# Performance work log

Hardware: AMD Instinct MI355X
Metric: run time of the kernel (lower is better)

Reference implementation:

```python
import jax, jax.numpy as jnp
import numpy as np

MUL0, MUL1 = 64, 32          # 64x0e + 32x1e irreps_emb
D_FEAT = MUL0 + 3 * MUL1     # 160
N_T, N_Q, N_K = 64, 1024, 1024


def quat_apply(q, v):
    # q: (...,4) real-first (w,x,y,z); v: (...,3). Rotate v by q.
    w = q[..., :1]
    u = q[..., 1:]
    uv = jnp.cross(u, v)
    return v + 2.0 * (w * uv + jnp.cross(u, uv))


def split_irreps(f):
    # f: (..., 160) -> scalars (...,64), vectors (...,32,3)
    s = f[..., :MUL0]
    v = f[..., MUL0:].reshape(f.shape[:-1] + (MUL1, 3))
    return s, v


def dtp(a, b, Ws, Wv):
    # Depthwise tensor product restricted to l<=1 (SeparableFCTP analogue),
    # output irreps 1x0e + 32x1e, with SiLU activation on the scalar part.
    sa, va = split_irreps(a)
    sb, vb = split_irreps(b)
    # scalar paths: 0e*0e and 1e.1e (dot) -> 96 scalar channels
    scal = jnp.concatenate([sa * sb, jnp.einsum('...ci,...ci->...c', va, vb)], axis=-1)
    # vector paths: 0e*1e, 1e*0e, 1e x 1e (cross) -> 96 vector channels
    vec = jnp.concatenate(
        [sa[..., :MUL1, None] * vb, va * sb[..., :MUL1, None], jnp.cross(va, vb)], axis=-2)
    out_s = jax.nn.silu(scal @ Ws)                    # (...,1)
    out_v = jnp.einsum('...ci,co->...oi', vec, Wv)    # (...,32,3)
    return out_s, out_v


def get_key_features(points, key_coord, key_feat, W_key):
    # radius-style key lookup: nearest key node + smooth radial envelope + linear
    d2 = jnp.sum((points[:, None, :] - key_coord[None, :, :]) ** 2, axis=-1)  # (M, N_K)
    idx = jnp.argmin(d2, axis=-1)
    dist = jnp.sqrt(jnp.take_along_axis(d2, idx[:, None], axis=1)[:, 0])
    env = jnp.exp(-dist)[:, None]
    return (key_feat[idx] * env) @ W_key              # (M, 160)


def setup_inputs() -> dict:
    key = jax.random.key(0)
    ks = jax.random.split(key, 11)
    return {
        'T': jax.random.normal(ks[0], (N_T, 7), jnp.float32),
        'query_weight': jax.random.uniform(ks[1], (N_Q,), jnp.float32),
        'query_feature': jax.random.normal(ks[2], (N_Q, D_FEAT), jnp.float32),
        'query_coord': jax.random.normal(ks[3], (N_Q, 3), jnp.float32),
        'key_coord': jax.random.normal(ks[4], (N_K, 3), jnp.float32),
        'key_node_feature': jax.random.normal(ks[5], (N_K, D_FEAT), jnp.float32),
        'W_key': jax.random.normal(ks[6], (D_FEAT, D_FEAT), jnp.float32) / np.sqrt(D_FEAT),
        'Ws_lin': jax.random.normal(ks[7], (96, 1), jnp.float32) / np.sqrt(96.0),
        'Wv_lin': jax.random.normal(ks[8], (96, 32), jnp.float32) / np.sqrt(96.0),
        'Ws_ang': jax.random.normal(ks[9], (96, 1), jnp.float32) / np.sqrt(96.0),
        'Wv_ang': jax.random.normal(ks[10], (96, 32), jnp.float32) / np.sqrt(96.0),
    }


def reference(T, query_weight, query_feature, query_coord, key_coord,
              key_node_feature, W_key, Ws_lin, Wv_lin, Ws_ang, Wv_ang):
    n_t = T.shape[0]
    n_q = query_feature.shape[0]
    q = T[:, :4]
    q = q / jnp.linalg.norm(q, axis=-1, keepdims=True)
    X = T[:, 4:]
    # transform query coords by each pose: (N_T, N_Q, 3)
    qc_t = quat_apply(q[:, None, :], query_coord[None, :, :]) + X[:, None, :]
    # equivariant feature transform: scalars unchanged, vectors rotated
    s, v = split_irreps(query_feature)
    v_t = quat_apply(q[:, None, None, :], v[None])                    # (N_T,N_Q,32,3)
    qf_t = jnp.concatenate(
        [jnp.broadcast_to(s, (n_t,) + s.shape), v_t.reshape(n_t, n_q, 3 * MUL1)],
        axis=-1).reshape(n_t * n_q, D_FEAT)
    # key feature gather over the expanded N_T*N_Q batch
    kf = get_key_features(qc_t.reshape(-1, 3), key_coord, key_node_feature, W_key)
    # two tensor products; original drops leading scalar ([..., 1:])
    _, lin = dtp(qf_t, kf, Ws_lin, Wv_lin)
    _, ang = dtp(qf_t, kf, Ws_ang, Wv_ang)
    lin = lin.reshape(n_t, n_q, MUL1, 3).mean(axis=-2)
    ang = ang.reshape(n_t, n_q, MUL1, 3).mean(axis=-2)
    # rotate back into body frame
    qinv = q * jnp.array([1.0, -1.0, -1.0, -1.0], q.dtype)
    lin = quat_apply(qinv[:, None, :], lin)
    ang = quat_apply(qinv[:, None, :], ang)
    ang_orbital = jnp.cross(query_coord[None], lin)
    lin_vel = jnp.einsum('q,tqi->ti', query_weight, lin)
    ang_vel = jnp.einsum('q,tqi->ti', query_weight, ang_orbital + ang)
    return lin_vel, ang_vel
```

## Files before the change

kernel.cpp:

```cpp
#include <hip/hip_runtime.h>
#include <math.h>

#define NT 64
#define NQ 1024
#define NK 1024
#define WS_KW 0
#define WS_QF 131072
#define WS_WV 262144

__launch_bounds__(256)
__global__ void prep_kernel(const float* __restrict__ qfeat,
                            const float* __restrict__ keyfeat,
                            const float* __restrict__ Wkey,
                            const float* __restrict__ WvL,
                            const float* __restrict__ WvA,
                            float* __restrict__ ws,
                            float* __restrict__ out) {
  const int blk = blockIdx.x;
  const int tid = threadIdx.x;
  if (blk < 128) {
    const int g = blk * 256 + tid;
    const int r = g >> 5;
    const int c = g & 31;
    const float* kf = keyfeat + r * 160;
    const int c0 = 64 + 3 * c;
    float a0 = 0.f, a1 = 0.f, a2 = 0.f, a3 = 0.f;
#pragma unroll 4
    for (int k = 0; k < 160; ++k) {
      const float f = kf[k];
      const float* wr = Wkey + k * 160;
      a0 = fmaf(f, wr[c0 + 0], a0);
      a1 = fmaf(f, wr[c0 + 1], a1);
      a2 = fmaf(f, wr[c0 + 2], a2);
      a3 = fmaf(f, wr[c], a3);
    }
    reinterpret_cast<float4*>(ws + WS_KW)[g] = make_float4(a0, a1, a2, a3);
  } else if (blk < 256) {
    const int g = (blk - 128) * 256 + tid;
    const int p = g >> 5;
    const int c = g & 31;
    const float* q = qfeat + p * 160;
    float4 o = make_float4(q[64 + 3 * c], q[65 + 3 * c], q[66 + 3 * c], q[c]);
    reinterpret_cast<float4*>(ws + WS_QF)[c * 1024 + p] = o;
  } else {
    out[tid] = 0.f;
    if (tid < 128) out[256 + tid] = 0.f;
    if (tid < 32) {
      const int c = tid;
      float m0 = 0.f, m1 = 0.f, m2 = 0.f, m3 = 0.f, m4 = 0.f, m5 = 0.f;
      for (int o = 0; o < 32; ++o) {
        m0 += WvL[c * 32 + o];
        m1 += WvL[(32 + c) * 32 + o];
        m2 += WvL[(64 + c) * 32 + o];
        m3 += WvA[c * 32 + o];
        m4 += WvA[(32 + c) * 32 + o];
        m5 += WvA[(64 + c) * 32 + o];
      }
      float* wv = ws + WS_WV + c * 8;
      const float s = 1.0f / 32.0f;
      wv[0] = m0 * s; wv[1] = m1 * s; wv[2] = m2 * s;
      wv[3] = m3 * s; wv[4] = m4 * s; wv[5] = m5 * s;
      wv[6] = 0.f; wv[7] = 0.f;
    }
  }
}

__launch_bounds__(256)
__global__ void main_kernel(const float* __restrict__ T,
                            const float* __restrict__ qweight,
                            const float* __restrict__ qcoord,
                            const float* __restrict__ kcoord,
                            const float* __restrict__ ws,
                            float* __restrict__ out) {
  __shared__ float4 keys[1024];
  __shared__ float red[4][8];
  const int tid = threadIdx.x;
  const int t = blockIdx.x >> 2;
  const int p = (blockIdx.x & 3) * 256 + tid;

  const float* Tt = T + t * 7;
  float qw = Tt[0], qx = Tt[1], qy = Tt[2], qz = Tt[3];
  const float Xx = Tt[4], Xy = Tt[5], Xz = Tt[6];
  const float rn = rsqrtf(qw * qw + qx * qx + qy * qy + qz * qz);
  qw *= rn; qx *= rn; qy *= rn; qz *= rn;
  const float ix = -qx, iy = -qy, iz = -qz;

  for (int j = 0; j < 4; ++j) {
    const int k = j * 256 + tid;
    keys[k] = make_float4(kcoord[k * 3 + 0], kcoord[k * 3 + 1], kcoord[k * 3 + 2], 0.f);
  }
  __syncthreads();

  const float qpx = qcoord[p * 3 + 0];
  const float qpy = qcoord[p * 3 + 1];
  const float qpz = qcoord[p * 3 + 2];

  const float uvx0 = qy * qpz - qz * qpy;
  const float uvy0 = qz * qpx - qx * qpz;
  const float uvz0 = qx * qpy - qy * qpx;
  const float qcx = qpx + 2.0f * (qw * uvx0 + (qy * uvz0 - qz * uvy0)) + Xx;
  const float qcy = qpy + 2.0f * (qw * uvy0 + (qz * uvx0 - qx * uvz0)) + Xy;
  const float qcz = qpz + 2.0f * (qw * uvz0 + (qx * uvy0 - qy * uvx0)) + Xz;

  float mv0 = 1e30f, mv1 = 1e30f;
  int mi0 = 0, mi1 = 0;
#pragma unroll 8
  for (int k = 0; k < 1024; k += 2) {
    const float4 K0 = keys[k];
    const float4 K1 = keys[k + 1];
    const float dx0 = qcx - K0.x, dy0 = qcy - K0.y, dz0 = qcz - K0.z;
    const float dx1 = qcx - K1.x, dy1 = qcy - K1.y, dz1 = qcz - K1.z;
    const float d0 = dx0 * dx0 + dy0 * dy0 + dz0 * dz0;
    const float d1 = dx1 * dx1 + dy1 * dy1 + dz1 * dz1;
    if (d0 < mv0) { mv0 = d0; mi0 = k; }
    if (d1 < mv1) { mv1 = d1; mi1 = k + 1; }
  }
  float mind2; int minidx;
  if (mv1 < mv0) { mind2 = mv1; minidx = mi1; }
  else           { mind2 = mv0; minidx = mi0; }

  const float env = expf(-sqrtf(mind2));

  const float4* kwrow = reinterpret_cast<const float4*>(ws + WS_KW) + minidx * 32;
  const float4* qfp   = reinterpret_cast<const float4*>(ws + WS_QF) + p;
  const float* wv = ws + WS_WV;
  float lx = 0.f, ly = 0.f, lz = 0.f, ax = 0.f, ay = 0.f, az = 0.f;
#pragma unroll 4
  for (int c = 0; c < 32; ++c) {
    const float4 B = kwrow[c];
    const float4 A = qfp[c * 1024];
    const float uvx = iy * B.z - iz * B.y;
    const float uvy = iz * B.x - ix * B.z;
    const float uvz = ix * B.y - iy * B.x;
    const float bx = B.x + 2.0f * (qw * uvx + (iy * uvz - iz * uvy));
    const float by = B.y + 2.0f * (qw * uvy + (iz * uvx - ix * uvz));
    const float bz = B.z + 2.0f * (qw * uvz + (ix * uvy - iy * uvx));
    const float crx = A.y * bz - A.z * by;
    const float cry = A.z * bx - A.x * bz;
    const float crz = A.x * by - A.y * bx;
    const float* w6 = wv + c * 8;
    const float a1L = w6[0] * A.w, a2L = w6[1] * B.w, w3L = w6[2];
    const float a1A = w6[3] * A.w, a2A = w6[4] * B.w, w3A = w6[5];
    lx = fmaf(a1L, bx, fmaf(a2L, A.x, fmaf(w3L, crx, lx)));
    ly = fmaf(a1L, by, fmaf(a2L, A.y, fmaf(w3L, cry, ly)));
    lz = fmaf(a1L, bz, fmaf(a2L, A.z, fmaf(w3L, crz, lz)));
    ax = fmaf(a1A, bx, fmaf(a2A, A.x, fmaf(w3A, crx, ax)));
    ay = fmaf(a1A, by, fmaf(a2A, A.y, fmaf(w3A, cry, ay)));
    az = fmaf(a1A, bz, fmaf(a2A, A.z, fmaf(w3A, crz, az)));
  }
  lx *= env; ly *= env; lz *= env;
  ax *= env; ay *= env; az *= env;

  const float wp = qweight[p];
  const float ox = qpy * lz - qpz * ly;
  const float oy = qpz * lx - qpx * lz;
  const float oz = qpx * ly - qpy * lx;
  float r0 = wp * lx, r1 = wp * ly, r2 = wp * lz;
  float r3 = wp * (ox + ax), r4 = wp * (oy + ay), r5 = wp * (oz + az);

#pragma unroll
  for (int m = 32; m >= 1; m >>= 1) {
    r0 += __shfl_xor(r0, m);
    r1 += __shfl_xor(r1, m);
    r2 += __shfl_xor(r2, m);
    r3 += __shfl_xor(r3, m);
    r4 += __shfl_xor(r4, m);
    r5 += __shfl_xor(r5, m);
  }
  const int wave = tid >> 6;
  const int lane = tid & 63;
  if (lane == 0) {
    red[wave][0] = r0; red[wave][1] = r1; red[wave][2] = r2;
    red[wave][3] = r3; red[wave][4] = r4; red[wave][5] = r5;
  }
  __syncthreads();
  if (tid < 6) {
    const float s = red[0][tid] + red[1][tid] + red[2][tid] + red[3][tid];
    const int row = (tid < 3) ? (t * 3 + tid) : (192 + t * 3 + (tid - 3));
    atomicAdd(out + row, s);
  }
}

extern "C" void kernel_launch(void* const* d_in, const int* in_sizes, int n_in,
                              void* d_out, int out_size, void* d_ws, size_t ws_size,
                              hipStream_t stream) {
  const float* T   = (const float*)d_in[0];
  const float* qw  = (const float*)d_in[1];
  const float* qf  = (const float*)d_in[2];
  const float* qc  = (const float*)d_in[3];
  const float* kc  = (const float*)d_in[4];
  const float* kf  = (const float*)d_in[5];
  const float* Wk  = (const float*)d_in[6];
  const float* WvL = (const float*)d_in[8];
  const float* WvA = (const float*)d_in[10];
  float* out = (float*)d_out;
  float* ws  = (float*)d_ws;

  prep_kernel<<<257, 256, 0, stream>>>(qf, kf, Wk, WvL, WvA, ws, out);
  main_kernel<<<256, 256, 0, stream>>>(T, qw, qc, kc, ws, out);
}
```

Baseline: 122.1 us.

## Split each query's key search and channel loop across four lanes

Each query point is now handled by four threads instead of one. Each thread scans a strided quarter of the keys and a quarter of the 32 channels, and the partial results are combined with xor shuffles, including a tie-break on index. The grid grows from 256 to 1024 blocks so more waves cover the GPU's CUs and the serial argmin loop gets shorter. In exchange, each block reloads the shared key array and per-query setup work is repeated across four lanes. The final sum is scaled by 0.25 because all four lanes contribute the same reduced value.

```diff
diff --git a/kernel.cpp b/kernel.cpp
--- a/kernel.cpp
+++ b/kernel.cpp
@@ -75,8 +75,10 @@
   __shared__ float4 keys[1024];
   __shared__ float red[4][8];
   const int tid = threadIdx.x;
-  const int t = blockIdx.x >> 2;
-  const int p = (blockIdx.x & 3) * 256 + tid;
+  const int t   = blockIdx.x >> 4;
+  const int pg  = blockIdx.x & 15;
+  const int p   = pg * 64 + (tid >> 2);
+  const int sub = tid & 3;
 
   const float* Tt = T + t * 7;
   float qw = Tt[0], qx = Tt[1], qy = Tt[2], qz = Tt[3];
@@ -105,28 +107,36 @@
   float mv0 = 1e30f, mv1 = 1e30f;
   int mi0 = 0, mi1 = 0;
 #pragma unroll 8
-  for (int k = 0; k < 1024; k += 2) {
-    const float4 K0 = keys[k];
-    const float4 K1 = keys[k + 1];
+  for (int m = 0; m < 256; m += 2) {
+    const int k0 = sub + 4 * m;
+    const int k1 = k0 + 4;
+    const float4 K0 = keys[k0];
+    const float4 K1 = keys[k1];
     const float dx0 = qcx - K0.x, dy0 = qcy - K0.y, dz0 = qcz - K0.z;
     const float dx1 = qcx - K1.x, dy1 = qcy - K1.y, dz1 = qcz - K1.z;
     const float d0 = dx0 * dx0 + dy0 * dy0 + dz0 * dz0;
     const float d1 = dx1 * dx1 + dy1 * dy1 + dz1 * dz1;
-    if (d0 < mv0) { mv0 = d0; mi0 = k; }
-    if (d1 < mv1) { mv1 = d1; mi1 = k + 1; }
-  }
-  float mind2; int minidx;
-  if (mv1 < mv0) { mind2 = mv1; minidx = mi1; }
-  else           { mind2 = mv0; minidx = mi0; }
-
-  const float env = expf(-sqrtf(mind2));
+    if (d0 < mv0) { mv0 = d0; mi0 = k0; }
+    if (d1 < mv1) { mv1 = d1; mi1 = k1; }
+  }
+  float mv = mv0; int mi = mi0;
+  if (mv1 < mv || (mv1 == mv && mi1 < mi)) { mv = mv1; mi = mi1; }
+#pragma unroll
+  for (int msk = 1; msk <= 2; msk <<= 1) {
+    const float vo = __shfl_xor(mv, msk);
+    const int   io = __shfl_xor(mi, msk);
+    if (vo < mv || (vo == mv && io < mi)) { mv = vo; mi = io; }
+  }
+  const int minidx = mi;
+  const float env = expf(-sqrtf(mv));
 
   const float4* kwrow = reinterpret_cast<const float4*>(ws + WS_KW) + minidx * 32;
   const float4* qfp   = reinterpret_cast<const float4*>(ws + WS_QF) + p;
   const float* wv = ws + WS_WV;
   float lx = 0.f, ly = 0.f, lz = 0.f, ax = 0.f, ay = 0.f, az = 0.f;
-#pragma unroll 4
-  for (int c = 0; c < 32; ++c) {
+#pragma unroll
+  for (int jj = 0; jj < 8; ++jj) {
+    const int c = 4 * jj + sub;
     const float4 B = kwrow[c];
     const float4 A = qfp[c * 1024];
     const float uvx = iy * B.z - iz * B.y;
@@ -148,6 +158,11 @@
     ay = fmaf(a1A, by, fmaf(a2A, A.y, fmaf(w3A, cry, ay)));
     az = fmaf(a1A, bz, fmaf(a2A, A.z, fmaf(w3A, crz, az)));
   }
+#pragma unroll
+  for (int msk = 1; msk <= 2; msk <<= 1) {
+    lx += __shfl_xor(lx, msk); ly += __shfl_xor(ly, msk); lz += __shfl_xor(lz, msk);
+    ax += __shfl_xor(ax, msk); ay += __shfl_xor(ay, msk); az += __shfl_xor(az, msk);
+  }
   lx *= env; ly *= env; lz *= env;
   ax *= env; ay *= env; az *= env;
 
@@ -177,7 +192,7 @@
   if (tid < 6) {
     const float s = red[0][tid] + red[1][tid] + red[2][tid] + red[3][tid];
     const int row = (tid < 3) ? (t * 3 + tid) : (192 + t * 3 + (tid - 3));
-    atomicAdd(out + row, s);
+    atomicAdd(out + row, s * 0.25f);
   }
 }
 
@@ -197,5 +212,5 @@
   float* ws  = (float*)d_ws;
 
   prep_kernel<<<257, 256, 0, stream>>>(qf, kf, Wk, WvL, WvA, ws, out);
-  main_kernel<<<256, 256, 0, stream>>>(T, qw, qc, kc, ws, out);
+  main_kernel<<<1024, 256, 0, stream>>>(T, qw, qc, kc, ws, out);
 }
```

New measurement: 112.4 us. -8.0%, faster.
